# Optimization experiments

Hardware: AMD Instinct MI355X
Metric: run time of the kernel (lower is better)

Reference implementation:

```python
import jax, jax.numpy as jnp
import numpy as np

N_FILTERS = 1024
N_HEADS = 16


def setup_inputs() -> dict:
    key = jax.random.key(0)
    k1, k2, k3 = jax.random.split(key, 3)
    x = jax.random.normal(k1, (8, 1024, N_FILTERS), dtype=jnp.float32)
    # VarianceScaling(0.02) ~ small dense init; 0.02*sqrt(1/fan_in) scale approximated
    w_qkv = jax.random.normal(k2, (N_FILTERS, N_FILTERS * 3), dtype=jnp.float32) * (0.02 / N_FILTERS) ** 0.5
    w_out = jax.random.normal(k3, (N_FILTERS, N_FILTERS), dtype=jnp.float32) * (0.02 / N_FILTERS) ** 0.5
    return {"x": x, "w_qkv": w_qkv, "w_out": w_out}


def reference(x, w_qkv, w_out):
    b, n, c = x.shape
    h = N_HEADS
    d = c // h
    qkv = jnp.einsum('bnc,ce->bne', x, w_qkv)  # [b, n, 3c]
    q, k, v = jnp.split(qkv, 3, axis=-1)
    # b n (h d) -> b h n d
    to_heads = lambda t: t.reshape(b, n, h, d).transpose(0, 2, 1, 3)
    q, k, v = to_heads(q), to_heads(k), to_heads(v)
    scale = jnp.sqrt(jnp.asarray(c, jnp.float32))  # NOTE: sqrt(n_filters), matches source
    attn = jnp.einsum('bhnd,bhmd->bhnm', q, k) / scale
    attn = jax.nn.softmax(attn, axis=-1)
    out = jnp.einsum('bhnm,bhmd->bhnd', attn, v)
    out = out.transpose(0, 2, 1, 3).reshape(b, n, c)  # b h n d -> b n (h d)
    return jnp.einsum('bnc,co->bno', out, w_out)
```

## Files before the change

### kernel.cpp

```cpp
#include <hip/hip_runtime.h>
#include <hip/hip_bf16.h>

typedef __bf16 bf16_t;
typedef __bf16 bf16x8 __attribute__((ext_vector_type(8)));
typedef __bf16 bf16x4 __attribute__((ext_vector_type(4)));
typedef float f32x4 __attribute__((ext_vector_type(4)));

constexpr int LD = 3072;

#define MFMA_16x16x32(a, b, c) __builtin_amdgcn_mfma_f32_16x16x32_bf16((a), (b), (c), 0, 0, 0)

#define GLOAD_LDS16(g, l)                                               \
  __builtin_amdgcn_global_load_lds(                                     \
      (const __attribute__((address_space(1))) void*)(g),               \
      (__attribute__((address_space(3))) void*)(l), 16, 0, 0)

#define TRREAD(dst, addr, imm) \
  asm volatile("ds_read_b64_tr_b16 %0, %1 offset:" imm : "=v"(dst) : "v"(addr))

__global__ void cvt_kernel(const float* __restrict__ in, bf16_t* __restrict__ out, int n8) {
  int i = blockIdx.x * blockDim.x + threadIdx.x;
  if (i >= n8) return;
  const float4 a = reinterpret_cast<const float4*>(in)[2 * i];
  const float4 c = reinterpret_cast<const float4*>(in)[2 * i + 1];
  bf16x8 o;
  o[0] = (bf16_t)a.x; o[1] = (bf16_t)a.y; o[2] = (bf16_t)a.z; o[3] = (bf16_t)a.w;
  o[4] = (bf16_t)c.x; o[5] = (bf16_t)c.y; o[6] = (bf16_t)c.z; o[7] = (bf16_t)c.w;
  reinterpret_cast<bf16x8*>(out)[i] = o;
}

__global__ void tcvt_kernel(const float* __restrict__ in, bf16_t* __restrict__ out, int R, int C) {
  __shared__ float tile[32][33];
  const int c0 = blockIdx.x * 32, r0 = blockIdx.y * 32;
  const int tx = threadIdx.x & 31, ty = threadIdx.x >> 5;
#pragma unroll
  for (int i = 0; i < 32; i += 8)
    tile[ty + i][tx] = in[(size_t)(r0 + ty + i) * C + (c0 + tx)];
  __syncthreads();
#pragma unroll
  for (int i = 0; i < 32; i += 8)
    out[(size_t)(c0 + ty + i) * R + (r0 + tx)] = (bf16_t)tile[tx][ty + i];
}

template <typename OutT>
__global__ __launch_bounds__(256) void gemm_bt_kernel(
    const bf16_t* __restrict__ A, const bf16_t* __restrict__ Bt, OutT* __restrict__ C,
    int M, int N, int K, int q_cols, float q_scale) {
  __shared__ bf16_t As[2][4096];
  __shared__ bf16_t Bs[2][4096];
  const int tid = threadIdx.x;
  const int lane = tid & 63;
  const int wave = tid >> 6;
  const int l15 = lane & 15, lg = lane >> 4;
  const int wr = wave >> 1, wc = wave & 1;
  const int brow = blockIdx.y * 128, bcol = blockIdx.x * 128;

  f32x4 acc[4][4] = {};

  const int srow = tid >> 2;
  const int scol = (tid & 3) * 8;
  const bf16_t* Ag = A + (size_t)(brow + srow) * K + scol;
  const bf16_t* Bg = Bt + (size_t)(bcol + srow) * K + scol;

  {
    bf16_t* aw = &As[0][wave * 512];
    bf16_t* bw = &Bs[0][wave * 512];
    GLOAD_LDS16(Ag, aw);
    GLOAD_LDS16(Ag + (size_t)64 * K, aw + 2048);
    GLOAD_LDS16(Bg, bw);
    GLOAD_LDS16(Bg + (size_t)64 * K, bw + 2048);
  }
  __syncthreads();

  const int nsteps = K >> 5;
  for (int i = 0; i < nsteps; i++) {
    if (i + 1 < nsteps) {
      const int k0 = (i + 1) << 5;
      bf16_t* aw = &As[(i + 1) & 1][wave * 512];
      bf16_t* bw = &Bs[(i + 1) & 1][wave * 512];
      GLOAD_LDS16(Ag + k0, aw);
      GLOAD_LDS16(Ag + k0 + (size_t)64 * K, aw + 2048);
      GLOAD_LDS16(Bg + k0, bw);
      GLOAD_LDS16(Bg + k0 + (size_t)64 * K, bw + 2048);
    }
    const bf16_t* as = As[i & 1];
    const bf16_t* bs = Bs[i & 1];
    bf16x8 af[4], bfr[4];
#pragma unroll
    for (int j = 0; j < 4; j++)
      af[j] = *reinterpret_cast<const bf16x8*>(as + (wr * 64 + j * 16 + l15) * 32 + lg * 8);
#pragma unroll
    for (int j = 0; j < 4; j++)
      bfr[j] = *reinterpret_cast<const bf16x8*>(bs + (wc * 64 + j * 16 + l15) * 32 + lg * 8);
#pragma unroll
    for (int j = 0; j < 4; j++)
#pragma unroll
      for (int k = 0; k < 4; k++)
        acc[j][k] = MFMA_16x16x32(af[j], bfr[k], acc[j][k]);
    __syncthreads();
  }

  const float sc = (bcol < q_cols) ? q_scale : 1.0f;
#pragma unroll
  for (int i = 0; i < 4; i++)
#pragma unroll
    for (int j = 0; j < 4; j++)
#pragma unroll
      for (int r = 0; r < 4; r++) {
        const size_t row = (size_t)(brow + wr * 64 + i * 16 + lg * 4 + r);
        const size_t col = (size_t)(bcol + wc * 64 + j * 16 + l15);
        C[row * N + col] = (OutT)(acc[i][j][r] * sc);
      }
}

__device__ __forceinline__ unsigned pack_bf16_pair(float a, float b) {
  union { __hip_bfloat162 h; unsigned u; } c;
  c.h = __float22bfloat162_rn(float2{a, b});
  return c.u;
}

__global__ __launch_bounds__(256, 3) void attn_kernel(const bf16_t* __restrict__ qkv,
                                                      bf16_t* __restrict__ ctx) {
  __shared__ bf16_t Ks[2][4096];
  __shared__ bf16_t Vs[2][4096];
  const int tid = threadIdx.x, lane = tid & 63, wave = tid >> 6;
  const int l15 = lane & 15, lg = (lane >> 4) & 3;
  const int flat = blockIdx.x;
  const int xcd = flat & 7, rr = flat >> 3;
  const int qt = rr & 7;
  const int hb = xcd * 16 + (rr >> 3);
  const int h = hb & 15, b = hb >> 4;
  const size_t base = (size_t)b * 1024 * LD;
  const int qbase = qt * 128 + wave * 32;

  bf16x8 qa[2][2];
#pragma unroll
  for (int s = 0; s < 2; s++) {
    const bf16_t* qp = qkv + base + (size_t)(qbase + s * 16 + l15) * LD + h * 64 + lg * 8;
    qa[s][0] = *reinterpret_cast<const bf16x8*>(qp);
    qa[s][1] = *reinterpret_cast<const bf16x8*>(qp + 32);
  }

  const bf16_t* Kb = qkv + base + 1024 + h * 64;
  const bf16_t* Vb = qkv + base + 2048 + h * 64;

  const int krr = lane >> 3;
  const int kcc = (lane & 7) ^ krr;
  const bf16_t* ksrc0 = Kb + (size_t)(wave * 16 + krr) * LD + kcc * 8;
  const bf16_t* ksrc1 = ksrc0 + (size_t)8 * LD;

  const int vd0 = (lane & 1) * 8 + wave * 16;
  const int vkv = ((lane >> 1) & 3) + ((lane >> 3) & 3) * 4 + (lane >> 5) * 16;
  const bf16_t* vsrc0 = Vb + (size_t)vkv * LD + vd0;
  const bf16_t* vsrc1 = vsrc0 + (size_t)32 * LD;

  bf16_t* ksb = &Ks[0][0];
  bf16_t* vsb = &Vs[0][0];
  const char* ksr = (const char*)&Ks[0][0];
  const unsigned vs_byte =
      (unsigned)(size_t)(__attribute__((address_space(3))) void*)(&Vs[0][0]);
  const unsigned tr_lane = vs_byte + lane * 8;

  const int rx7 = l15 & 7;
  const unsigned kb0 = (unsigned)(l15 * 128 + ((lg ^ rx7) << 4));
  const unsigned kb1 = (unsigned)(l15 * 128 + (((4 | lg) ^ rx7) << 4));

  float lr[2] = {0.f, 0.f};
  f32x4 oacc[2][4] = {};

  GLOAD_LDS16(ksrc0, ksb + wave * 1024);
  GLOAD_LDS16(ksrc1, ksb + wave * 1024 + 512);
  GLOAD_LDS16(vsrc0, vsb + wave * 1024);
  GLOAD_LDS16(vsrc1, vsb + wave * 1024 + 512);
  ksrc0 += (size_t)64 * LD; ksrc1 += (size_t)64 * LD;
  vsrc0 += (size_t)64 * LD; vsrc1 += (size_t)64 * LD;
  __syncthreads();

  for (int t = 0; t < 16; t++) {
    const int cur = t & 1;
    if (t < 15) {
      bf16_t* kd = ksb + (cur ^ 1) * 4096 + wave * 1024;
      bf16_t* vd = vsb + (cur ^ 1) * 4096 + wave * 1024;
      GLOAD_LDS16(ksrc0, kd);
      GLOAD_LDS16(ksrc1, kd + 512);
      GLOAD_LDS16(vsrc0, vd);
      GLOAD_LDS16(vsrc1, vd + 512);
      ksrc0 += (size_t)64 * LD; ksrc1 += (size_t)64 * LD;
      vsrc0 += (size_t)64 * LD; vsrc1 += (size_t)64 * LD;
    }

    f32x4 sacc[2][4] = {};
    const char* kt = ksr + cur * 8192;
    __builtin_amdgcn_s_setprio(1);
#pragma unroll
    for (int tt = 0; tt < 4; tt++) {
      const bf16x8 k0 = *reinterpret_cast<const bf16x8*>(kt + tt * 2048 + kb0);
      const bf16x8 k1 = *reinterpret_cast<const bf16x8*>(kt + tt * 2048 + kb1);
      sacc[0][tt] = MFMA_16x16x32(k0, qa[0][0], sacc[0][tt]);
      sacc[0][tt] = MFMA_16x16x32(k1, qa[0][1], sacc[0][tt]);
      sacc[1][tt] = MFMA_16x16x32(k0, qa[1][0], sacc[1][tt]);
      sacc[1][tt] = MFMA_16x16x32(k1, qa[1][1], sacc[1][tt]);
    }
    __builtin_amdgcn_s_setprio(0);

    const unsigned ta = tr_lane + (unsigned)cur * 8192;
    bf16x4 tl0, th0, tl2, th2, tl4, th4, tl6, th6;
    TRREAD(tl0, ta, "0");    TRREAD(th0, ta, "512");
    TRREAD(tl2, ta, "2048"); TRREAD(th2, ta, "2560");
    TRREAD(tl4, ta, "4096"); TRREAD(th4, ta, "4608");
    TRREAD(tl6, ta, "6144"); TRREAD(th6, ta, "6656");
    __builtin_amdgcn_sched_barrier(0);

    unsigned pu[16];
    float ls0 = 0.f, ls1 = 0.f;
#pragma unroll
    for (int tt = 0; tt < 4; tt++) {
      const float a0 = __builtin_exp2f(sacc[0][tt][0]);
      const float a1 = __builtin_exp2f(sacc[0][tt][1]);
      const float a2 = __builtin_exp2f(sacc[0][tt][2]);
      const float a3 = __builtin_exp2f(sacc[0][tt][3]);
      ls0 += (a0 + a1) + (a2 + a3);
      pu[(tt >> 1) * 4 + (tt & 1) * 2 + 0] = pack_bf16_pair(a0, a1);
      pu[(tt >> 1) * 4 + (tt & 1) * 2 + 1] = pack_bf16_pair(a2, a3);
      const float b0 = __builtin_exp2f(sacc[1][tt][0]);
      const float b1 = __builtin_exp2f(sacc[1][tt][1]);
      const float b2 = __builtin_exp2f(sacc[1][tt][2]);
      const float b3 = __builtin_exp2f(sacc[1][tt][3]);
      ls1 += (b0 + b1) + (b2 + b3);
      pu[8 + (tt >> 1) * 4 + (tt & 1) * 2 + 0] = pack_bf16_pair(b0, b1);
      pu[8 + (tt >> 1) * 4 + (tt & 1) * 2 + 1] = pack_bf16_pair(b2, b3);
    }
    lr[0] += ls0;
    lr[1] += ls1;
    bf16x8 pa[2][2];
    pa[0][0] = *reinterpret_cast<bf16x8*>(&pu[0]);
    pa[0][1] = *reinterpret_cast<bf16x8*>(&pu[4]);
    pa[1][0] = *reinterpret_cast<bf16x8*>(&pu[8]);
    pa[1][1] = *reinterpret_cast<bf16x8*>(&pu[12]);

    bf16x4 tl1, th1, tl3, th3, tl5, th5, tl7, th7;
    TRREAD(tl1, ta, "1024"); TRREAD(th1, ta, "1536");
    TRREAD(tl3, ta, "3072"); TRREAD(th3, ta, "3584");
    TRREAD(tl5, ta, "5120"); TRREAD(th5, ta, "5632");
    TRREAD(tl7, ta, "7168"); TRREAD(th7, ta, "7680");

    asm volatile("s_waitcnt lgkmcnt(8)" ::: "memory");
    __builtin_amdgcn_sched_barrier(0);
    {
      bf16x8 vb0[4];
      vb0[0] = __builtin_shufflevector(tl0, th0, 0, 1, 2, 3, 4, 5, 6, 7);
      vb0[1] = __builtin_shufflevector(tl2, th2, 0, 1, 2, 3, 4, 5, 6, 7);
      vb0[2] = __builtin_shufflevector(tl4, th4, 0, 1, 2, 3, 4, 5, 6, 7);
      vb0[3] = __builtin_shufflevector(tl6, th6, 0, 1, 2, 3, 4, 5, 6, 7);
      __builtin_amdgcn_s_setprio(1);
#pragma unroll
      for (int s = 0; s < 2; s++)
#pragma unroll
        for (int dt = 0; dt < 4; dt++)
          oacc[s][dt] = MFMA_16x16x32(pa[s][0], vb0[dt], oacc[s][dt]);
      __builtin_amdgcn_s_setprio(0);
    }

    asm volatile("s_waitcnt lgkmcnt(0)" ::: "memory");
    __builtin_amdgcn_sched_barrier(0);
    {
      bf16x8 vb1[4];
      vb1[0] = __builtin_shufflevector(tl1, th1, 0, 1, 2, 3, 4, 5, 6, 7);
      vb1[1] = __builtin_shufflevector(tl3, th3, 0, 1, 2, 3, 4, 5, 6, 7);
      vb1[2] = __builtin_shufflevector(tl5, th5, 0, 1, 2, 3, 4, 5, 6, 7);
      vb1[3] = __builtin_shufflevector(tl7, th7, 0, 1, 2, 3, 4, 5, 6, 7);
      __builtin_amdgcn_s_setprio(1);
#pragma unroll
      for (int s = 0; s < 2; s++)
#pragma unroll
        for (int dt = 0; dt < 4; dt++)
          oacc[s][dt] = MFMA_16x16x32(pa[s][1], vb1[dt], oacc[s][dt]);
      __builtin_amdgcn_s_setprio(0);
    }

    __syncthreads();
  }

#pragma unroll
  for (int s = 0; s < 2; s++) {
    float v = lr[s];
    v += __shfl_xor(v, 16);
    v += __shfl_xor(v, 32);
#pragma unroll
    for (int r = 0; r < 4; r++) {
      const float inv = 1.0f / __shfl(v, lg * 4 + r);
      const size_t row = (size_t)(b * 1024 + qbase + s * 16 + lg * 4 + r);
#pragma unroll
      for (int dt = 0; dt < 4; dt++)
        ctx[row * 1024 + h * 64 + dt * 16 + l15] = (bf16_t)(oacc[s][dt][r] * inv);
    }
  }
}

extern "C" void kernel_launch(void* const* d_in, const int* in_sizes, int n_in,
                              void* d_out, int out_size, void* d_ws, size_t ws_size,
                              hipStream_t stream) {
  (void)in_sizes; (void)n_in; (void)out_size; (void)ws_size;
  const float* x = (const float*)d_in[0];
  const float* w_qkv = (const float*)d_in[1];
  const float* w_out = (const float*)d_in[2];
  float* out = (float*)d_out;
  char* ws = (char*)d_ws;

  bf16_t* x_b   = (bf16_t*)(ws);
  bf16_t* qkv_b = (bf16_t*)(ws + (size_t)(16 << 20));
  bf16_t* wqT   = (bf16_t*)(ws + (size_t)(64 << 20));
  bf16_t* woT   = (bf16_t*)(ws + (size_t)(70 << 20));
  bf16_t* ctx_b = (bf16_t*)(ws + (size_t)(72 << 20));

  const float qsc = 0.045084220027780106f;

  cvt_kernel<<<8388608 / 8 / 256, 256, 0, stream>>>(x, x_b, 8388608 / 8);
  tcvt_kernel<<<dim3(3072 / 32, 1024 / 32), 256, 0, stream>>>(w_qkv, wqT, 1024, 3072);
  tcvt_kernel<<<dim3(1024 / 32, 1024 / 32), 256, 0, stream>>>(w_out, woT, 1024, 1024);

  gemm_bt_kernel<bf16_t><<<dim3(3072 / 128, 8192 / 128), 256, 0, stream>>>(
      x_b, wqT, qkv_b, 8192, 3072, 1024, 1024, qsc);
  attn_kernel<<<1024, 256, 0, stream>>>(qkv_b, ctx_b);
  gemm_bt_kernel<float><<<dim3(1024 / 128, 8192 / 128), 256, 0, stream>>>(
      ctx_b, woT, out, 8192, 1024, 1024, 0, 1.0f);
}
```

Measured before the change: 177.5 us.

## Add 256x256-tile QKV GEMM kernel with interleaved LDS staging and MFMA schedule

Replaces the generic 128x128 QKV projection GEMM with a dedicated kernel. It uses 256x256 output tiles, 512 threads (8 waves) and 128 KB of double-buffered, XOR-swizzled dynamic LDS. Global-to-LDS loads for the next K-tile are split into quarters and interleaved with MFMA phases, separated by explicit barriers and lgkmcnt waits, with raised wave priority during the MFMAs. Block IDs are remapped so tiles are grouped per XCD. The goal is more data reuse per loaded byte and better overlap of loads with compute. The trade-offs are a grid of only 384 large blocks, which leaves an uneven tail over the CUs, and a 128 KB dynamic LDS request that may need an explicit launch attribute.

```diff
diff --git a/kernel.cpp b/kernel.cpp
--- a/kernel.cpp
+++ b/kernel.cpp
@@ -17,6 +17,10 @@
 
 #define TRREAD(dst, addr, imm) \
   asm volatile("ds_read_b64_tr_b16 %0, %1 offset:" imm : "=v"(dst) : "v"(addr))
+
+#define BAR __builtin_amdgcn_s_barrier()
+#define LGKM0 do { asm volatile("s_waitcnt lgkmcnt(0)" ::: "memory"); \
+                   __builtin_amdgcn_sched_barrier(0); } while (0)
 
 __global__ void cvt_kernel(const float* __restrict__ in, bf16_t* __restrict__ out, int n8) {
   int i = blockIdx.x * blockDim.x + threadIdx.x;
@@ -40,6 +44,129 @@
 #pragma unroll
   for (int i = 0; i < 32; i += 8)
     out[(size_t)(c0 + ty + i) * R + (r0 + tx)] = (bf16_t)tile[tx][ty + i];
+}
+
+__global__ __launch_bounds__(512, 2) void gemm_qkv_256(
+    const bf16_t* __restrict__ A, const bf16_t* __restrict__ Bt,
+    bf16_t* __restrict__ C, float q_scale) {
+  constexpr int K = 1024;
+  extern __shared__ char smem[];
+  char* asB = smem;
+  char* bsB = smem + 65536;
+
+  const int t = threadIdx.x;
+  const int lane = t & 63, wave = t >> 6;
+  const int l15 = lane & 15, lg = lane >> 4;
+  const int wr = wave >> 2, wc = wave & 3;
+
+  const int bid = blockIdx.x;
+  const int wg = (bid & 7) * 48 + (bid >> 3);
+  const int brow = (wg & 31) * 256;
+  const int bcol = (wg >> 5) * 256;
+
+  const int srow = t >> 3;
+  const int schk = (t & 7) ^ (srow & 7);
+  const bf16_t* aS = A + (size_t)(brow + srow) * K + schk * 8;
+  const bf16_t* bS = Bt + (size_t)(bcol + srow) * K + schk * 8;
+  const int ldst = t * 8;
+
+#define STG_A(T, H) do {                                                      \
+    const bf16_t* _s = aS + (size_t)((H) * 128) * K + (T) * 64;               \
+    bf16_t* _d = (bf16_t*)(asB + ((T) & 1) * 32768 + (H) * 16384) + ldst;     \
+    GLOAD_LDS16(_s, _d);                                                      \
+    GLOAD_LDS16(_s + (size_t)64 * K, _d + 4096);                              \
+  } while (0)
+#define STG_B(T, H) do {                                                      \
+    const bf16_t* _s = bS + (size_t)((H) * 128) * K + (T) * 64;               \
+    bf16_t* _d = (bf16_t*)(bsB + ((T) & 1) * 32768 + (H) * 16384) + ldst;     \
+    GLOAD_LDS16(_s, _d);                                                      \
+    GLOAD_LDS16(_s + (size_t)64 * K, _d + 4096);                              \
+  } while (0)
+
+  const int rx = l15 & 7;
+  const unsigned c0 = ((unsigned)(lg ^ rx)) << 4;
+  const unsigned c1 = ((unsigned)((4 | lg) ^ rx)) << 4;
+  const unsigned a_rd = (unsigned)(wr * 16384 + l15 * 128);
+  const unsigned b_rd = (unsigned)((wc >> 1) * 16384 + (wc & 1) * 8192 + l15 * 128);
+
+  f32x4 acc[8][4] = {};
+  bf16x8 af[4][2], bfr[2][2];
+
+#define RD_AF(BUF, MH) do { _Pragma("unroll")                                 \
+    for (int m = 0; m < 4; ++m) {                                             \
+      const char* _p = asB + (BUF) * 32768 + a_rd + ((MH) * 4 + m) * 2048;    \
+      af[m][0] = *(const bf16x8*)(_p + c0);                                   \
+      af[m][1] = *(const bf16x8*)(_p + c1); } } while (0)
+#define RD_BF(BUF, NH) do { _Pragma("unroll")                                 \
+    for (int n = 0; n < 2; ++n) {                                             \
+      const char* _p = bsB + (BUF) * 32768 + b_rd + ((NH) * 2 + n) * 2048;    \
+      bfr[n][0] = *(const bf16x8*)(_p + c0);                                  \
+      bfr[n][1] = *(const bf16x8*)(_p + c1); } } while (0)
+#define MM16(MH, NH) do {                                                     \
+    __builtin_amdgcn_s_setprio(1);                                            \
+    _Pragma("unroll")                                                         \
+    for (int m = 0; m < 4; ++m) { _Pragma("unroll")                           \
+      for (int n = 0; n < 2; ++n) {                                           \
+        acc[(MH)*4+m][(NH)*2+n] =                                             \
+            MFMA_16x16x32(af[m][0], bfr[n][0], acc[(MH)*4+m][(NH)*2+n]);      \
+        acc[(MH)*4+m][(NH)*2+n] =                                             \
+            MFMA_16x16x32(af[m][1], bfr[n][1], acc[(MH)*4+m][(NH)*2+n]); } }  \
+    __builtin_amdgcn_s_setprio(0); } while (0)
+
+  STG_A(0, 0); STG_A(0, 1); STG_B(0, 0); STG_B(0, 1); STG_A(1, 0);
+  asm volatile("s_waitcnt vmcnt(2)" ::: "memory");
+  BAR;
+
+  for (int i = 0; i < 8; ++i) {
+    const int T1 = 2 * i + 1, T2 = 2 * i + 2, T3 = 2 * i + 3;
+    const bool pf = (i < 7);
+    STG_A(T1, 1);
+    RD_AF(0, 0); RD_BF(0, 0);
+    BAR; LGKM0; MM16(0, 0); BAR;
+    STG_B(T1, 0);
+    RD_BF(0, 1);
+    BAR; LGKM0; MM16(0, 1); BAR;
+    STG_B(T1, 1);
+    RD_AF(0, 1);
+    BAR; LGKM0; MM16(1, 1); BAR;
+    if (pf) STG_A(T2, 0);
+    RD_BF(0, 0);
+    BAR; LGKM0; MM16(1, 0);
+    if (pf) asm volatile("s_waitcnt vmcnt(2)" ::: "memory");
+    else    asm volatile("s_waitcnt vmcnt(0)" ::: "memory");
+    BAR;
+    if (pf) STG_A(T2, 1);
+    RD_AF(1, 0); RD_BF(1, 0);
+    BAR; LGKM0; MM16(0, 0); BAR;
+    if (pf) STG_B(T2, 0);
+    RD_BF(1, 1);
+    BAR; LGKM0; MM16(0, 1); BAR;
+    if (pf) STG_B(T2, 1);
+    RD_AF(1, 1);
+    BAR; LGKM0; MM16(1, 1); BAR;
+    if (pf) STG_A(T3, 0);
+    RD_BF(1, 0);
+    BAR; LGKM0; MM16(1, 0);
+    asm volatile("s_waitcnt vmcnt(2)" ::: "memory");
+    BAR;
+  }
+
+  const float sc = (bcol < 1024) ? q_scale : 1.0f;
+  const int crow0 = brow + wr * 128 + lg * 4;
+  const int ccol0 = bcol + wc * 64 + l15;
+#pragma unroll
+  for (int m = 0; m < 8; ++m)
+#pragma unroll
+    for (int n = 0; n < 4; ++n)
+#pragma unroll
+      for (int r = 0; r < 4; ++r)
+        C[(size_t)(crow0 + m * 16 + r) * 3072 + ccol0 + n * 16] =
+            (bf16_t)(acc[m][n][r] * sc);
+#undef STG_A
+#undef STG_B
+#undef RD_AF
+#undef RD_BF
+#undef MM16
 }
 
 template <typename OutT>
@@ -319,8 +446,7 @@
   tcvt_kernel<<<dim3(3072 / 32, 1024 / 32), 256, 0, stream>>>(w_qkv, wqT, 1024, 3072);
   tcvt_kernel<<<dim3(1024 / 32, 1024 / 32), 256, 0, stream>>>(w_out, woT, 1024, 1024);
 
-  gemm_bt_kernel<bf16_t><<<dim3(3072 / 128, 8192 / 128), 256, 0, stream>>>(
-      x_b, wqT, qkv_b, 8192, 3072, 1024, 1024, qsc);
+  gemm_qkv_256<<<384, 512, 131072, stream>>>(x_b, wqT, qkv_b, qsc);
   attn_kernel<<<1024, 256, 0, stream>>>(qkv_b, ctx_b);
   gemm_bt_kernel<float><<<dim3(1024 / 128, 8192 / 128), 256, 0, stream>>>(
       ctx_b, woT, out, 8192, 1024, 1024, 0, 1.0f);
```

Result: faster. 169.9 us (-4.3%).

## Replace GEMM with 128x256-tile, 512-thread, triple-buffered swizzled kernel

Applied to the files above, without the earlier changes.

Both projection GEMMs move from a 128x128 tile, 256-thread, double-buffered kernel with K-step 32 to a 128x256 tile, 8-wave kernel with K-step 64. It uses three LDS stages in 144KB of dynamic shared memory, an XOR-swizzled LDS layout to avoid bank conflicts, and an XCD-aware block remap. The split prefetch and MFMA phases with explicit waitcnt/barriers and setprio aim to overlap global loads with matrix math and raise per-block reuse. In exchange it hardcodes K=1024, runs one block per CU, and leaves a small grid (256 blocks) for the output projection.

```diff
diff --git a/kernel.cpp b/kernel.cpp
--- a/kernel.cpp
+++ b/kernel.cpp
@@ -17,6 +17,10 @@
 
 #define TRREAD(dst, addr, imm) \
   asm volatile("ds_read_b64_tr_b16 %0, %1 offset:" imm : "=v"(dst) : "v"(addr))
+
+#define BAR __builtin_amdgcn_s_barrier()
+#define LGKM0 do { asm volatile("s_waitcnt lgkmcnt(0)" ::: "memory"); \
+                   __builtin_amdgcn_sched_barrier(0); } while (0)
 
 __global__ void cvt_kernel(const float* __restrict__ in, bf16_t* __restrict__ out, int n8) {
   int i = blockIdx.x * blockDim.x + threadIdx.x;
@@ -43,74 +47,112 @@
 }
 
 template <typename OutT>
-__global__ __launch_bounds__(256) void gemm_bt_kernel(
-    const bf16_t* __restrict__ A, const bf16_t* __restrict__ Bt, OutT* __restrict__ C,
-    int M, int N, int K, int q_cols, float q_scale) {
-  __shared__ bf16_t As[2][4096];
-  __shared__ bf16_t Bs[2][4096];
-  const int tid = threadIdx.x;
-  const int lane = tid & 63;
-  const int wave = tid >> 6;
+__global__ __launch_bounds__(512, 1) void gemm_bt_128x256(
+    const bf16_t* __restrict__ A, const bf16_t* __restrict__ Bt,
+    OutT* __restrict__ C, int N, int nrowblk, int q_cols, float q_scale) {
+  constexpr int K = 1024;
+  extern __shared__ char smem[];
+  char* asB = smem;
+  char* bsB = smem + 49152;
+
+  const int t = threadIdx.x;
+  const int lane = t & 63, wave = t >> 6;
   const int l15 = lane & 15, lg = lane >> 4;
-  const int wr = wave >> 1, wc = wave & 1;
-  const int brow = blockIdx.y * 128, bcol = blockIdx.x * 128;
+  const int wr = wave >> 2, wc = wave & 3;
+
+  const int cpx = (int)gridDim.x >> 3;
+  const int bid = blockIdx.x;
+  const int wg = (bid & 7) * cpx + (bid >> 3);
+  const int brow = (wg % nrowblk) * 128;
+  const int bcol = (wg / nrowblk) * 256;
+
+  const int srow = t >> 3;
+  const int schk = (t & 7) ^ (srow & 7);
+  const bf16_t* aS = A + (size_t)(brow + srow) * K + schk * 8;
+  const bf16_t* bS = Bt + (size_t)(bcol + srow) * K + schk * 8;
+  const int ldst = t * 8;
+
+#define STG_A(T, BUF) do {                                               \
+    const bf16_t* _s = aS + (T) * 64;                                    \
+    bf16_t* _d = (bf16_t*)(asB + (BUF) * 16384) + ldst;                  \
+    GLOAD_LDS16(_s, _d);                                                 \
+    GLOAD_LDS16(_s + (size_t)64 * K, _d + 4096);                         \
+  } while (0)
+#define STG_B(T, H, BUF) do {                                            \
+    const bf16_t* _s = bS + (size_t)((H) * 128) * K + (T) * 64;          \
+    bf16_t* _d = (bf16_t*)(bsB + (BUF) * 32768 + (H) * 16384) + ldst;    \
+    GLOAD_LDS16(_s, _d);                                                 \
+    GLOAD_LDS16(_s + (size_t)64 * K, _d + 4096);                         \
+  } while (0)
+
+  const int rx = l15 & 7;
+  const unsigned c0 = ((unsigned)(lg ^ rx)) << 4;
+  const unsigned c1 = ((unsigned)((4 | lg) ^ rx)) << 4;
+  const unsigned a_rd = (unsigned)(wr * 8192 + l15 * 128);
+  const unsigned b_rd = (unsigned)((wc >> 1) * 16384 + (wc & 1) * 8192 + l15 * 128);
 
   f32x4 acc[4][4] = {};
-
-  const int srow = tid >> 2;
-  const int scol = (tid & 3) * 8;
-  const bf16_t* Ag = A + (size_t)(brow + srow) * K + scol;
-  const bf16_t* Bg = Bt + (size_t)(bcol + srow) * K + scol;
-
-  {
-    bf16_t* aw = &As[0][wave * 512];
-    bf16_t* bw = &Bs[0][wave * 512];
-    GLOAD_LDS16(Ag, aw);
-    GLOAD_LDS16(Ag + (size_t)64 * K, aw + 2048);
-    GLOAD_LDS16(Bg, bw);
-    GLOAD_LDS16(Bg + (size_t)64 * K, bw + 2048);
+  bf16x8 af[2][2], bfr[4][2];
+
+#define RD_AF(BUF, MH) do { _Pragma("unroll")                            \
+    for (int m = 0; m < 2; ++m) {                                        \
+      const char* _p = asB + (BUF) * 16384 + a_rd + ((MH) * 2 + m) * 2048; \
+      af[m][0] = *(const bf16x8*)(_p + c0);                              \
+      af[m][1] = *(const bf16x8*)(_p + c1); } } while (0)
+#define RD_BF(BUF) do { _Pragma("unroll")                                \
+    for (int n = 0; n < 4; ++n) {                                        \
+      const char* _p = bsB + (BUF) * 32768 + b_rd + n * 2048;            \
+      bfr[n][0] = *(const bf16x8*)(_p + c0);                             \
+      bfr[n][1] = *(const bf16x8*)(_p + c1); } } while (0)
+#define MM(MH) do {                                                      \
+    __builtin_amdgcn_s_setprio(1);                                       \
+    _Pragma("unroll")                                                    \
+    for (int m = 0; m < 2; ++m) { _Pragma("unroll")                      \
+      for (int n = 0; n < 4; ++n) {                                      \
+        acc[(MH)*2+m][n] =                                               \
+            MFMA_16x16x32(af[m][0], bfr[n][0], acc[(MH)*2+m][n]);        \
+        acc[(MH)*2+m][n] =                                               \
+            MFMA_16x16x32(af[m][1], bfr[n][1], acc[(MH)*2+m][n]); } }    \
+    __builtin_amdgcn_s_setprio(0); } while (0)
+
+  STG_A(0, 0); STG_B(0, 0, 0); STG_B(0, 1, 0);
+  STG_A(1, 1); STG_B(1, 0, 1); STG_B(1, 1, 1);
+  asm volatile("s_waitcnt vmcnt(6)" ::: "memory");
+  BAR;
+
+  int bc = 0;
+  for (int T = 0; T < 16; ++T) {
+    const bool pf = (T + 2 < 16);
+    const int bs = (bc >= 1) ? (bc - 1) : 2;
+    if (pf) { STG_A(T + 2, bs); STG_B(T + 2, 0, bs); }
+    RD_AF(bc, 0);
+    RD_BF(bc);
+    BAR; LGKM0; MM(0); BAR;
+    if (pf) STG_B(T + 2, 1, bs);
+    RD_AF(bc, 1);
+    BAR; LGKM0; MM(1);
+    if (pf) asm volatile("s_waitcnt vmcnt(6)" ::: "memory");
+    else    asm volatile("s_waitcnt vmcnt(0)" ::: "memory");
+    BAR;
+    bc = (bc == 2) ? 0 : bc + 1;
   }
-  __syncthreads();
-
-  const int nsteps = K >> 5;
-  for (int i = 0; i < nsteps; i++) {
-    if (i + 1 < nsteps) {
-      const int k0 = (i + 1) << 5;
-      bf16_t* aw = &As[(i + 1) & 1][wave * 512];
-      bf16_t* bw = &Bs[(i + 1) & 1][wave * 512];
-      GLOAD_LDS16(Ag + k0, aw);
-      GLOAD_LDS16(Ag + k0 + (size_t)64 * K, aw + 2048);
-      GLOAD_LDS16(Bg + k0, bw);
-      GLOAD_LDS16(Bg + k0 + (size_t)64 * K, bw + 2048);
-    }
-    const bf16_t* as = As[i & 1];
-    const bf16_t* bs = Bs[i & 1];
-    bf16x8 af[4], bfr[4];
-#pragma unroll
-    for (int j = 0; j < 4; j++)
-      af[j] = *reinterpret_cast<const bf16x8*>(as + (wr * 64 + j * 16 + l15) * 32 + lg * 8);
-#pragma unroll
-    for (int j = 0; j < 4; j++)
-      bfr[j] = *reinterpret_cast<const bf16x8*>(bs + (wc * 64 + j * 16 + l15) * 32 + lg * 8);
-#pragma unroll
-    for (int j = 0; j < 4; j++)
-#pragma unroll
-      for (int k = 0; k < 4; k++)
-        acc[j][k] = MFMA_16x16x32(af[j], bfr[k], acc[j][k]);
-    __syncthreads();
-  }
 
   const float sc = (bcol < q_cols) ? q_scale : 1.0f;
-#pragma unroll
-  for (int i = 0; i < 4; i++)
-#pragma unroll
-    for (int j = 0; j < 4; j++)
-#pragma unroll
-      for (int r = 0; r < 4; r++) {
-        const size_t row = (size_t)(brow + wr * 64 + i * 16 + lg * 4 + r);
-        const size_t col = (size_t)(bcol + wc * 64 + j * 16 + l15);
-        C[row * N + col] = (OutT)(acc[i][j][r] * sc);
-      }
+  const int crow0 = brow + wr * 64 + lg * 4;
+  const int ccol0 = bcol + wc * 64 + l15;
+#pragma unroll
+  for (int m = 0; m < 4; ++m)
+#pragma unroll
+    for (int n = 0; n < 4; ++n)
+#pragma unroll
+      for (int r = 0; r < 4; ++r)
+        C[(size_t)(crow0 + m * 16 + r) * N + ccol0 + n * 16] =
+            (OutT)(acc[m][n][r] * sc);
+#undef STG_A
+#undef STG_B
+#undef RD_AF
+#undef RD_BF
+#undef MM
 }
 
 __device__ __forceinline__ unsigned pack_bf16_pair(float a, float b) {
@@ -319,9 +361,9 @@
   tcvt_kernel<<<dim3(3072 / 32, 1024 / 32), 256, 0, stream>>>(w_qkv, wqT, 1024, 3072);
   tcvt_kernel<<<dim3(1024 / 32, 1024 / 32), 256, 0, stream>>>(w_out, woT, 1024, 1024);
 
-  gemm_bt_kernel<bf16_t><<<dim3(3072 / 128, 8192 / 128), 256, 0, stream>>>(
-      x_b, wqT, qkv_b, 8192, 3072, 1024, 1024, qsc);
+  gemm_bt_128x256<bf16_t><<<768, 512, 147456, stream>>>(
+      x_b, wqT, qkv_b, 3072, 64, 1024, qsc);
   attn_kernel<<<1024, 256, 0, stream>>>(qkv_b, ctx_b);
-  gemm_bt_kernel<float><<<dim3(1024 / 128, 8192 / 128), 256, 0, stream>>>(
-      ctx_b, woT, out, 8192, 1024, 1024, 0, 1.0f);
-}
+  gemm_bt_128x256<float><<<256, 512, 147456, stream>>>(
+      ctx_b, woT, out, 1024, 64, 0, 1.0f);
+}
```

Result: faster. 168.0 us (-5.3%).
